# Kernel tuning notes

Measured on AMD Instinct MI355X. Metric: run time of the kernel, lower is better.

Reference implementation:

```python
import jax, jax.numpy as jnp
import numpy as np

N = 16384
D = 16          # chem_dims
K = 17          # knn k (first neighbor = self, dropped)
N_LAYERS = 3
NEG_SLOPE = 0.2
EPS = 1e-5


def group_norm(m, gamma, beta, groups=2, eps=EPS):
    # m: [N, C]; torch GroupNorm normalizes each row over each channel group
    n, c = m.shape
    g = m.reshape(n, groups, c // groups)
    mu = g.mean(-1, keepdims=True)
    var = ((g - mu) ** 2).mean(-1, keepdims=True)
    g = (g - mu) / jnp.sqrt(var + eps)
    return g.reshape(n, c) * gamma + beta


def setup_inputs() -> dict:
    key = jax.random.key(0)
    ks = jax.random.split(key, 8)
    x = jax.random.normal(ks[0], (N, 3), dtype=jnp.float32) * 10.0
    y = x  # atom-atom self graph: same point cloud
    y_atomtypes = jax.random.normal(ks[1], (N, D), dtype=jnp.float32)
    x_batch = jnp.sort(jax.random.randint(ks[2], (N,), 0, 4)).astype(jnp.int32)
    y_batch = x_batch
    Din = 2 * D + 1  # 33
    W1 = jax.random.normal(ks[3], (N_LAYERS, Din, Din), dtype=jnp.float32) * 0.1
    b1 = jnp.zeros((N_LAYERS, Din), dtype=jnp.float32)
    W2 = jax.random.normal(ks[4], (N_LAYERS, Din, D), dtype=jnp.float32) * 0.1
    b2 = jnp.zeros((N_LAYERS, D), dtype=jnp.float32)
    gamma = jnp.ones((N_LAYERS, D), dtype=jnp.float32)
    beta = jnp.zeros((N_LAYERS, D), dtype=jnp.float32)
    return {"x": x, "y": y, "y_atomtypes": y_atomtypes, "W1": W1, "b1": b1,
            "W2": W2, "b2": b2, "gamma": gamma, "beta": beta,
            "x_batch": x_batch, "y_batch": y_batch}


def knn(x, y, x_batch, y_batch, k):
    # brute-force batched KNN (keops argKmin equivalent)
    d2 = ((x * x).sum(-1)[:, None] + (y * y).sum(-1)[None, :]
          - 2.0 * x @ y.T)                                  # [N, N]
    d2 = jnp.where(x_batch[:, None] != y_batch[None, :], jnp.float32(1e30), d2)
    _, idx = jax.lax.top_k(-d2, k)                          # smallest distances
    return idx


def reference(x, y, y_atomtypes, W1, b1, W2, b2, gamma, beta, x_batch, y_batch):
    idx = knn(x, y, x_batch, y_batch, K)[:, 1:]             # drop self -> [N, K-1]
    nbr_xyz = y[idx]                                        # [N, k, 3]
    dists = ((x[:, None, :] - nbr_xyz) ** 2).sum(-1)        # [N, k]
    k = K - 1
    out = y_atomtypes
    for i in range(N_LAYERS):
        nbr = out[idx]                                      # [N, k, D] gather
        feat = jnp.concatenate(
            [jnp.broadcast_to(out[:, None, :], (out.shape[0], k, out.shape[1])),
             nbr, dists[..., None]], axis=-1)               # [N, k, 2D+1]
        h = jax.nn.leaky_relu(feat @ W1[i] + b1[i], NEG_SLOPE)
        messages = (h @ W2[i] + b2[i]).sum(1)               # sum over k -> [N, D]
        out = out + jax.nn.leaky_relu(group_norm(messages, gamma[i], beta[i]), NEG_SLOPE)
    return out
```

## Files before the change

### kernel.cpp

```cpp
#include <hip/hip_runtime.h>


#define N_PTS 16384
#define D 16
#define DIN 33
#define NEG 0.2f
#define GEPS 1e-5f
#define INFF 3.0e38f
#define SHRINK_AT 192

__global__ __launch_bounds__(256) void prep_kernel(const float* __restrict__ x,
                                                   float4* __restrict__ xyz4, int n) {
  int i = blockIdx.x * 256 + threadIdx.x;
  if (i < n) xyz4[i] = make_float4(x[3*i], x[3*i+1], x[3*i+2], 0.f);
}

__device__ __forceinline__ int pool_shrink(float* __restrict__ pd, int* __restrict__ pi,
                                           int pcount, float& tau, int l,
                                           unsigned long long lmask) {
  __asm__ volatile("s_waitcnt lgkmcnt(0)" ::: "memory");
  float e0 = INFF, e1 = INFF, e2 = INFF, e3 = INFF;
  int   j0 = 0, j1 = 0, j2 = 0, j3 = 0;
  const bool p0 = l < pcount, p1 = l + 64 < pcount, p2 = l + 128 < pcount, p3 = l + 192 < pcount;
  if (p0) { e0 = pd[l];       j0 = pi[l]; }
  if (p1) { e1 = pd[l + 64];  j1 = pi[l + 64]; }
  if (p2) { e2 = pd[l + 128]; j2 = pi[l + 128]; }
  if (p3) { e3 = pd[l + 192]; j3 = pi[l + 192]; }
  float mx = fmaxf(fmaxf(p0 ? e0 : 0.f, p1 ? e1 : 0.f), fmaxf(p2 ? e2 : 0.f, p3 ? e3 : 0.f));
#pragma unroll
  for (int m = 1; m < 64; m <<= 1) mx = fmaxf(mx, __shfl_xor(mx, m));
  float lo = 0.f, hi = mx * 1.000001f + 1e-35f;
  for (int it = 0; it < 12; ++it) {
    const float mid = 0.5f * (lo + hi);
    const int c = __popcll(__ballot(e0 < mid)) + __popcll(__ballot(e1 < mid))
                + __popcll(__ballot(e2 < mid)) + __popcll(__ballot(e3 < mid));
    if (c >= 16) hi = mid; else lo = mid;
  }
  tau = hi;
  int base = 0;
  { const bool k = e0 < tau; const unsigned long long m = __ballot(k);
    if (k) { const int pos = base + __popcll(m & lmask); pd[pos] = e0; pi[pos] = j0; }
    base += __popcll(m); }
  { const bool k = e1 < tau; const unsigned long long m = __ballot(k);
    if (k) { const int pos = base + __popcll(m & lmask); pd[pos] = e1; pi[pos] = j1; }
    base += __popcll(m); }
  { const bool k = e2 < tau; const unsigned long long m = __ballot(k);
    if (k) { const int pos = base + __popcll(m & lmask); pd[pos] = e2; pi[pos] = j2; }
    base += __popcll(m); }
  { const bool k = e3 < tau; const unsigned long long m = __ballot(k);
    if (k) { const int pos = base + __popcll(m & lmask); pd[pos] = e3; pi[pos] = j3; }
    base += __popcll(m); }
  return base;
}

__device__ __forceinline__ void pool_extract16(const float* __restrict__ pd,
                                               const int* __restrict__ pi,
                                               int pcount, int q, int l,
                                               int* __restrict__ knn_idx,
                                               float* __restrict__ knn_d2) {
  __asm__ volatile("s_waitcnt lgkmcnt(0)" ::: "memory");
  float e0 = INFF, e1 = INFF, e2 = INFF, e3 = INFF;
  int   j0 = -1 - l, j1 = -65 - l, j2 = -129 - l, j3 = -193 - l;
  if (l       < pcount) { e0 = pd[l];       j0 = pi[l]; }
  if (l + 64  < pcount) { e1 = pd[l + 64];  j1 = pi[l + 64]; }
  if (l + 128 < pcount) { e2 = pd[l + 128]; j2 = pi[l + 128]; }
  if (l + 192 < pcount) { e3 = pd[l + 192]; j3 = pi[l + 192]; }
  float rv = 0.f; int ri = q;
  for (int r = 0; r < 16; ++r) {
    float bv = e0; int bi = j0; int bs = 0;
    if (e1 < bv || (e1 == bv && j1 < bi)) { bv = e1; bi = j1; bs = 1; }
    if (e2 < bv || (e2 == bv && j2 < bi)) { bv = e2; bi = j2; bs = 2; }
    if (e3 < bv || (e3 == bv && j3 < bi)) { bv = e3; bi = j3; bs = 3; }
    const float lv = bv; const int li = bi;
#pragma unroll
    for (int m = 1; m < 64; m <<= 1) {
      const float ov = __shfl_xor(bv, m);
      const int   oi = __shfl_xor(bi, m);
      if (ov < bv || (ov == bv && oi < bi)) { bv = ov; bi = oi; }
    }
    if (lv == bv && li == bi) {
      if (bs == 0)      { e0 = INFF; j0 = -1 - l; }
      else if (bs == 1) { e1 = INFF; j1 = -65 - l; }
      else if (bs == 2) { e2 = INFF; j2 = -129 - l; }
      else              { e3 = INFF; j3 = -193 - l; }
    }
    if (l == r) { rv = bv; ri = bi; }
  }
  if (l < 16) {
    knn_idx[q * 16 + l] = ri;
    knn_d2 [q * 16 + l] = rv;
  }
}

__global__ __launch_bounds__(256) void knn_kernel(const float4* __restrict__ xyz4,
                                                  const int* __restrict__ batch,
                                                  int* __restrict__ knn_idx,
                                                  float* __restrict__ knn_d2, int n) {
  __shared__ float pd[4][256];
  __shared__ int   pi[4][256];
  const int tid = threadIdx.x;
  const int w = tid >> 6;
  const int l = tid & 63;
  const int q = blockIdx.x * 4 + w;

  const float4 Q = xyz4[q];
  const int b = batch[q];
  int lo, hi;
  { int a = 0, c = n; while (a < c) { int m = (a + c) >> 1; if (batch[m] <  b) a = m + 1; else c = m; } lo = a; }
  { int a = lo, c = n; while (a < c) { int m = (a + c) >> 1; if (batch[m] <= b) a = m + 1; else c = m; } hi = a; }

  const unsigned long long lmask = (1ull << l) - 1ull;
  float tau = INFF;
  int pcount = 0;

  for (int j0 = lo; j0 < hi; j0 += 64) {
    const int j = j0 + l;
    bool pass = false; float d2 = 0.f;
    if (j < hi) {
      const float4 P = xyz4[j];
      const float dx = Q.x - P.x, dy = Q.y - P.y, dz = Q.z - P.z;
      d2 = dx*dx + dy*dy + dz*dz;
      pass = (d2 < tau) && (j != q);
    }
    const unsigned long long m = __ballot(pass);
    if (m) {
      if (pass) {
        const int pos = pcount + __popcll(m & lmask);
        pd[w][pos] = d2; pi[w][pos] = j;
      }
      pcount += __popcll(m);
      if (pcount >= SHRINK_AT) {
        pcount = pool_shrink(&pd[w][0], &pi[w][0], pcount, tau, l, lmask);
      }
    }
  }
  pool_extract16(&pd[w][0], &pi[w][0], pcount, q, l, knn_idx, knn_d2);
}

__device__ __forceinline__ void load16(const float4* __restrict__ base, int row, float* dst) {
  float4 a = base[row*4+0], b = base[row*4+1], c = base[row*4+2], d = base[row*4+3];
  dst[0]=a.x;  dst[1]=a.y;  dst[2]=a.z;  dst[3]=a.w;
  dst[4]=b.x;  dst[5]=b.y;  dst[6]=b.z;  dst[7]=b.w;
  dst[8]=c.x;  dst[9]=c.y;  dst[10]=c.z; dst[11]=c.w;
  dst[12]=d.x; dst[13]=d.y; dst[14]=d.z; dst[15]=d.w;
}

__device__ __forceinline__ float lrelu(float x) {
  return fmaxf(x, 0.f) + NEG * fminf(x, 0.f);
}

__global__ __launch_bounds__(256) void layer_kernel(
    const float* __restrict__ in, const int* __restrict__ knn_idx,
    const float* __restrict__ knn_d2,
    const float* __restrict__ W1, const float* __restrict__ b1,
    const float* __restrict__ W2, const float* __restrict__ b2,
    const float* __restrict__ gamma, const float* __restrict__ beta,
    float* __restrict__ outb) {
  __shared__ float sW2[DIN * D];
  __shared__ float sb2[D], sg[D], sbt[D];
  const int tid = threadIdx.x;
  for (int t = tid; t < DIN * D; t += 256) sW2[t] = W2[t];
  if (tid < D) { sb2[tid] = b2[tid]; sg[tid] = gamma[tid]; sbt[tid] = beta[tid]; }
  __syncthreads();

  const int p = blockIdx.x * 16 + (tid >> 4);
  const int c = tid & 15;
  const float4* in4 = (const float4*)in;

  float s[16], nf[16];
  load16(in4, p, s);
  const int   nb = knn_idx[p * 16 + c];
  const float dk = knn_d2 [p * 16 + c];
  load16(in4, nb, nf);

  float h[DIN];
#pragma unroll
  for (int o = 0; o < DIN; ++o) h[o] = b1[o] + dk * W1[32 * DIN + o];
#pragma unroll
  for (int i = 0; i < 16; ++i) {
    const float si = s[i], ni = nf[i];
#pragma unroll
    for (int o = 0; o < DIN; ++o) {
      h[o] += si * W1[i * DIN + o];
      h[o] += ni * W1[(16 + i) * DIN + o];
    }
  }
#pragma unroll
  for (int o = 0; o < DIN; ++o) h[o] = lrelu(h[o]);

#pragma unroll
  for (int o = 0; o < DIN; ++o) {
    float x = h[o];
    x += __shfl_xor(x, 1);
    x += __shfl_xor(x, 2);
    x += __shfl_xor(x, 4);
    x += __shfl_xor(x, 8);
    h[o] = x;
  }

  float m = sb2[c];
#pragma unroll
  for (int i = 0; i < DIN; ++i) m += h[i] * sW2[i * D + c];

  float sum = m;
  sum += __shfl_xor(sum, 1); sum += __shfl_xor(sum, 2); sum += __shfl_xor(sum, 4);
  const float mu = sum * 0.125f;
  const float dd = m - mu;
  float sq = dd * dd;
  sq += __shfl_xor(sq, 1); sq += __shfl_xor(sq, 2); sq += __shfl_xor(sq, 4);
  const float var = sq * 0.125f;
  float yv = dd * (1.0f / sqrtf(var + GEPS));
  yv = yv * sg[c] + sbt[c];

  const float selfc = in[p * 16 + c];
  outb[p * 16 + c] = selfc + lrelu(yv);
}

extern "C" void kernel_launch(void* const* d_in, const int* in_sizes, int n_in,
                              void* d_out, int out_size, void* d_ws, size_t ws_size,
                              hipStream_t stream) {
  const float* x     = (const float*)d_in[0];
  const float* yat   = (const float*)d_in[2];
  const float* W1    = (const float*)d_in[3];
  const float* b1    = (const float*)d_in[4];
  const float* W2    = (const float*)d_in[5];
  const float* b2    = (const float*)d_in[6];
  const float* gamma = (const float*)d_in[7];
  const float* beta  = (const float*)d_in[8];
  const int*   xb    = (const int*)d_in[9];
  float* out = (float*)d_out;

  char* ws = (char*)d_ws;
  float4* xyz4 = (float4*)(ws);
  int*    kidx = (int*)  (ws + 262144);
  float*  kd2  = (float*)(ws + 262144 + 1048576);
  float*  bufA = (float*)(ws + 262144 + 2*1048576);
  float*  bufB = (float*)(ws + 262144 + 3*1048576);

  prep_kernel<<<N_PTS / 256, 256, 0, stream>>>(x, xyz4, N_PTS);
  knn_kernel<<<N_PTS / 4, 256, 0, stream>>>(xyz4, xb, kidx, kd2, N_PTS);
  layer_kernel<<<N_PTS / 16, 256, 0, stream>>>(yat,  kidx, kd2,
      W1 + 0*DIN*DIN, b1 + 0*DIN, W2 + 0*DIN*D, b2 + 0*D, gamma + 0*D, beta + 0*D, bufA);
  layer_kernel<<<N_PTS / 16, 256, 0, stream>>>(bufA, kidx, kd2,
      W1 + 1*DIN*DIN, b1 + 1*DIN, W2 + 1*DIN*D, b2 + 1*D, gamma + 1*D, beta + 1*D, bufB);
  layer_kernel<<<N_PTS / 16, 256, 0, stream>>>(bufB, kidx, kd2,
      W1 + 2*DIN*DIN, b1 + 2*DIN, W2 + 2*DIN*D, b2 + 2*D, gamma + 2*D, beta + 2*D, out);
}
```

Measured before the change: 234.3 us.

## Use integer-bit bisection for KNN selection and split layer work by output channel

```diff
diff --git a/kernel.cpp b/kernel.cpp
--- a/kernel.cpp
+++ b/kernel.cpp
@@ -7,6 +7,7 @@
 #define NEG 0.2f
 #define GEPS 1e-5f
 #define INFF 3.0e38f
+#define INFU 0x7f800000u
 #define SHRINK_AT 192
 
 __global__ __launch_bounds__(256) void prep_kernel(const float* __restrict__ x,
@@ -15,81 +16,98 @@
   if (i < n) xyz4[i] = make_float4(x[3*i], x[3*i+1], x[3*i+2], 0.f);
 }
 
+__device__ __forceinline__ unsigned bisect16(unsigned u0, unsigned u1,
+                                             unsigned u2, unsigned u3) {
+  unsigned lo = 0u, hi = 0x7f800001u;
+  for (int it = 0; it < 31; ++it) {
+    const unsigned mid = lo + ((hi - lo) >> 1);
+    const int c = __popcll(__ballot(u0 < mid)) + __popcll(__ballot(u1 < mid))
+                + __popcll(__ballot(u2 < mid)) + __popcll(__ballot(u3 < mid));
+    if (c >= 16) hi = mid; else lo = mid;
+  }
+  return lo;
+}
+
 __device__ __forceinline__ int pool_shrink(float* __restrict__ pd, int* __restrict__ pi,
                                            int pcount, float& tau, int l,
                                            unsigned long long lmask) {
   __asm__ volatile("s_waitcnt lgkmcnt(0)" ::: "memory");
-  float e0 = INFF, e1 = INFF, e2 = INFF, e3 = INFF;
-  int   j0 = 0, j1 = 0, j2 = 0, j3 = 0;
-  const bool p0 = l < pcount, p1 = l + 64 < pcount, p2 = l + 128 < pcount, p3 = l + 192 < pcount;
-  if (p0) { e0 = pd[l];       j0 = pi[l]; }
-  if (p1) { e1 = pd[l + 64];  j1 = pi[l + 64]; }
-  if (p2) { e2 = pd[l + 128]; j2 = pi[l + 128]; }
-  if (p3) { e3 = pd[l + 192]; j3 = pi[l + 192]; }
-  float mx = fmaxf(fmaxf(p0 ? e0 : 0.f, p1 ? e1 : 0.f), fmaxf(p2 ? e2 : 0.f, p3 ? e3 : 0.f));
-#pragma unroll
-  for (int m = 1; m < 64; m <<= 1) mx = fmaxf(mx, __shfl_xor(mx, m));
-  float lo = 0.f, hi = mx * 1.000001f + 1e-35f;
-  for (int it = 0; it < 12; ++it) {
-    const float mid = 0.5f * (lo + hi);
-    const int c = __popcll(__ballot(e0 < mid)) + __popcll(__ballot(e1 < mid))
-                + __popcll(__ballot(e2 < mid)) + __popcll(__ballot(e3 < mid));
-    if (c >= 16) hi = mid; else lo = mid;
-  }
-  tau = hi;
+  unsigned u0 = INFU, u1 = INFU, u2 = INFU, u3 = INFU;
+  int j0 = 0, j1 = 0, j2 = 0, j3 = 0;
+  if (l       < pcount) { u0 = __float_as_uint(pd[l]);       j0 = pi[l]; }
+  if (l + 64  < pcount) { u1 = __float_as_uint(pd[l + 64]);  j1 = pi[l + 64]; }
+  if (l + 128 < pcount) { u2 = __float_as_uint(pd[l + 128]); j2 = pi[l + 128]; }
+  if (l + 192 < pcount) { u3 = __float_as_uint(pd[l + 192]); j3 = pi[l + 192]; }
+  const unsigned t = bisect16(u0, u1, u2, u3);
+  tau = __uint_as_float(t);
   int base = 0;
-  { const bool k = e0 < tau; const unsigned long long m = __ballot(k);
-    if (k) { const int pos = base + __popcll(m & lmask); pd[pos] = e0; pi[pos] = j0; }
-    base += __popcll(m); }
-  { const bool k = e1 < tau; const unsigned long long m = __ballot(k);
-    if (k) { const int pos = base + __popcll(m & lmask); pd[pos] = e1; pi[pos] = j1; }
-    base += __popcll(m); }
-  { const bool k = e2 < tau; const unsigned long long m = __ballot(k);
-    if (k) { const int pos = base + __popcll(m & lmask); pd[pos] = e2; pi[pos] = j2; }
-    base += __popcll(m); }
-  { const bool k = e3 < tau; const unsigned long long m = __ballot(k);
-    if (k) { const int pos = base + __popcll(m & lmask); pd[pos] = e3; pi[pos] = j3; }
+  { const bool k = u0 <= t; const unsigned long long m = __ballot(k);
+    if (k) { const int pos = base + __popcll(m & lmask);
+             pd[pos] = __uint_as_float(u0); pi[pos] = j0; }
+    base += __popcll(m); }
+  { const bool k = u1 <= t; const unsigned long long m = __ballot(k);
+    if (k) { const int pos = base + __popcll(m & lmask);
+             pd[pos] = __uint_as_float(u1); pi[pos] = j1; }
+    base += __popcll(m); }
+  { const bool k = u2 <= t; const unsigned long long m = __ballot(k);
+    if (k) { const int pos = base + __popcll(m & lmask);
+             pd[pos] = __uint_as_float(u2); pi[pos] = j2; }
+    base += __popcll(m); }
+  { const bool k = u3 <= t; const unsigned long long m = __ballot(k);
+    if (k) { const int pos = base + __popcll(m & lmask);
+             pd[pos] = __uint_as_float(u3); pi[pos] = j3; }
     base += __popcll(m); }
   return base;
 }
 
-__device__ __forceinline__ void pool_extract16(const float* __restrict__ pd,
-                                               const int* __restrict__ pi,
-                                               int pcount, int q, int l,
-                                               int* __restrict__ knn_idx,
-                                               float* __restrict__ knn_d2) {
+__device__ __forceinline__ void pool_final16(const float* __restrict__ pd,
+                                             const int* __restrict__ pi,
+                                             int pcount, int q, int l,
+                                             int* __restrict__ knn_idx,
+                                             float* __restrict__ knn_d2) {
   __asm__ volatile("s_waitcnt lgkmcnt(0)" ::: "memory");
-  float e0 = INFF, e1 = INFF, e2 = INFF, e3 = INFF;
-  int   j0 = -1 - l, j1 = -65 - l, j2 = -129 - l, j3 = -193 - l;
-  if (l       < pcount) { e0 = pd[l];       j0 = pi[l]; }
-  if (l + 64  < pcount) { e1 = pd[l + 64];  j1 = pi[l + 64]; }
-  if (l + 128 < pcount) { e2 = pd[l + 128]; j2 = pi[l + 128]; }
-  if (l + 192 < pcount) { e3 = pd[l + 192]; j3 = pi[l + 192]; }
-  float rv = 0.f; int ri = q;
-  for (int r = 0; r < 16; ++r) {
-    float bv = e0; int bi = j0; int bs = 0;
-    if (e1 < bv || (e1 == bv && j1 < bi)) { bv = e1; bi = j1; bs = 1; }
-    if (e2 < bv || (e2 == bv && j2 < bi)) { bv = e2; bi = j2; bs = 2; }
-    if (e3 < bv || (e3 == bv && j3 < bi)) { bv = e3; bi = j3; bs = 3; }
-    const float lv = bv; const int li = bi;
-#pragma unroll
-    for (int m = 1; m < 64; m <<= 1) {
-      const float ov = __shfl_xor(bv, m);
-      const int   oi = __shfl_xor(bi, m);
-      if (ov < bv || (ov == bv && oi < bi)) { bv = ov; bi = oi; }
-    }
-    if (lv == bv && li == bi) {
-      if (bs == 0)      { e0 = INFF; j0 = -1 - l; }
-      else if (bs == 1) { e1 = INFF; j1 = -65 - l; }
-      else if (bs == 2) { e2 = INFF; j2 = -129 - l; }
-      else              { e3 = INFF; j3 = -193 - l; }
-    }
-    if (l == r) { rv = bv; ri = bi; }
-  }
-  if (l < 16) {
-    knn_idx[q * 16 + l] = ri;
-    knn_d2 [q * 16 + l] = rv;
-  }
+  const unsigned long long lmask = (1ull << l) - 1ull;
+  unsigned u0 = INFU, u1 = INFU, u2 = INFU, u3 = INFU;
+  int j0 = 0, j1 = 0, j2 = 0, j3 = 0;
+  if (l       < pcount) { u0 = __float_as_uint(pd[l]);       j0 = pi[l]; }
+  if (l + 64  < pcount) { u1 = __float_as_uint(pd[l + 64]);  j1 = pi[l + 64]; }
+  if (l + 128 < pcount) { u2 = __float_as_uint(pd[l + 128]); j2 = pi[l + 128]; }
+  if (l + 192 < pcount) { u3 = __float_as_uint(pd[l + 192]); j3 = pi[l + 192]; }
+  const unsigned t = bisect16(u0, u1, u2, u3);
+  int base = 0;
+  { const bool k = u0 < t; const unsigned long long m = __ballot(k);
+    if (k) { const int pos = base + __popcll(m & lmask);
+             knn_idx[q*16+pos] = j0; knn_d2[q*16+pos] = __uint_as_float(u0); }
+    base += __popcll(m); }
+  { const bool k = u1 < t; const unsigned long long m = __ballot(k);
+    if (k) { const int pos = base + __popcll(m & lmask);
+             knn_idx[q*16+pos] = j1; knn_d2[q*16+pos] = __uint_as_float(u1); }
+    base += __popcll(m); }
+  { const bool k = u2 < t; const unsigned long long m = __ballot(k);
+    if (k) { const int pos = base + __popcll(m & lmask);
+             knn_idx[q*16+pos] = j2; knn_d2[q*16+pos] = __uint_as_float(u2); }
+    base += __popcll(m); }
+  { const bool k = u3 < t; const unsigned long long m = __ballot(k);
+    if (k) { const int pos = base + __popcll(m & lmask);
+             knn_idx[q*16+pos] = j3; knn_d2[q*16+pos] = __uint_as_float(u3); }
+    base += __popcll(m); }
+  const float tf = __uint_as_float(t);
+  { const bool k = u0 == t; const unsigned long long m = __ballot(k);
+    if (k) { const int pos = base + __popcll(m & lmask);
+             if (pos < 16) { knn_idx[q*16+pos] = j0; knn_d2[q*16+pos] = tf; } }
+    base += __popcll(m); }
+  { const bool k = u1 == t; const unsigned long long m = __ballot(k);
+    if (k) { const int pos = base + __popcll(m & lmask);
+             if (pos < 16) { knn_idx[q*16+pos] = j1; knn_d2[q*16+pos] = tf; } }
+    base += __popcll(m); }
+  { const bool k = u2 == t; const unsigned long long m = __ballot(k);
+    if (k) { const int pos = base + __popcll(m & lmask);
+             if (pos < 16) { knn_idx[q*16+pos] = j2; knn_d2[q*16+pos] = tf; } }
+    base += __popcll(m); }
+  { const bool k = u3 == t; const unsigned long long m = __ballot(k);
+    if (k) { const int pos = base + __popcll(m & lmask);
+             if (pos < 16) { knn_idx[q*16+pos] = j3; knn_d2[q*16+pos] = tf; } }
+    base += __popcll(m); }
 }
 
 __global__ __launch_bounds__(256) void knn_kernel(const float4* __restrict__ xyz4,
@@ -134,7 +152,7 @@
       }
     }
   }
-  pool_extract16(&pd[w][0], &pi[w][0], pcount, q, l, knn_idx, knn_d2);
+  pool_final16(&pd[w][0], &pi[w][0], pcount, q, l, knn_idx, knn_d2);
 }
 
 __device__ __forceinline__ void load16(const float4* __restrict__ base, int row, float* dst) {
@@ -156,51 +174,65 @@
     const float* __restrict__ W2, const float* __restrict__ b2,
     const float* __restrict__ gamma, const float* __restrict__ beta,
     float* __restrict__ outb) {
-  __shared__ float sW2[DIN * D];
-  __shared__ float sb2[D], sg[D], sbt[D];
   const int tid = threadIdx.x;
-  for (int t = tid; t < DIN * D; t += 256) sW2[t] = W2[t];
-  if (tid < D) { sb2[tid] = b2[tid]; sg[tid] = gamma[tid]; sbt[tid] = beta[tid]; }
-  __syncthreads();
-
-  const int p = blockIdx.x * 16 + (tid >> 4);
+  const int g = tid >> 4;
   const int c = tid & 15;
+  const int p = blockIdx.x * 16 + g;
+
+  __shared__ float sH[16][36];
+
+  float w1a[DIN], w1b[DIN], w2c[DIN];
+#pragma unroll
+  for (int i = 0; i < DIN; ++i) {
+    w1a[i] = W1[i*DIN + c];
+    w1b[i] = W1[i*DIN + 16 + c];
+    w2c[i] = W2[i*D + c];
+  }
+  const float b1a = b1[c], b1b = b1[16 + c];
+
   const float4* in4 = (const float4*)in;
-
-  float s[16], nf[16];
+  float s[16];
   load16(in4, p, s);
-  const int   nb = knn_idx[p * 16 + c];
-  const float dk = knn_d2 [p * 16 + c];
-  load16(in4, nb, nf);
-
-  float h[DIN];
-#pragma unroll
-  for (int o = 0; o < DIN; ++o) h[o] = b1[o] + dk * W1[32 * DIN + o];
-#pragma unroll
-  for (int i = 0; i < 16; ++i) {
-    const float si = s[i], ni = nf[i];
-#pragma unroll
-    for (int o = 0; o < DIN; ++o) {
-      h[o] += si * W1[i * DIN + o];
-      h[o] += ni * W1[(16 + i) * DIN + o];
-    }
-  }
-#pragma unroll
-  for (int o = 0; o < DIN; ++o) h[o] = lrelu(h[o]);
-
-#pragma unroll
-  for (int o = 0; o < DIN; ++o) {
-    float x = h[o];
-    x += __shfl_xor(x, 1);
-    x += __shfl_xor(x, 2);
-    x += __shfl_xor(x, 4);
-    x += __shfl_xor(x, 8);
-    h[o] = x;
-  }
-
-  float m = sb2[c];
-#pragma unroll
-  for (int i = 0; i < DIN; ++i) m += h[i] * sW2[i * D + c];
+
+  const int*   kidx = knn_idx + p * 16;
+  const float* kd2  = knn_d2  + p * 16;
+
+  float hsA = 0.f, hsB = 0.f, hsZ = 0.f;
+#pragma unroll 2
+  for (int k = 0; k < 16; ++k) {
+    const int   nb = kidx[k];
+    const float dk = kd2[k];
+    float nf[16];
+    load16(in4, nb, nf);
+    float ha = b1a + dk * w1a[32];
+    float hb = b1b + dk * w1b[32];
+#pragma unroll
+    for (int i = 0; i < 16; ++i) {
+      ha += s[i]  * w1a[i];
+      ha += nf[i] * w1a[16 + i];
+      hb += s[i]  * w1b[i];
+      hb += nf[i] * w1b[16 + i];
+    }
+    hsA += lrelu(ha);
+    hsB += lrelu(hb);
+    if (c == 15) {
+      float hz = b1[32] + dk * W1[32*DIN + 32];
+#pragma unroll
+      for (int i = 0; i < 16; ++i) {
+        hz += s[i]  * W1[i*DIN + 32];
+        hz += nf[i] * W1[(16 + i)*DIN + 32];
+      }
+      hsZ += lrelu(hz);
+    }
+  }
+
+  sH[g][c]      = hsA;
+  sH[g][16 + c] = hsB;
+  if (c == 15) sH[g][32] = hsZ;
+
+  float m = b2[c];
+#pragma unroll
+  for (int i = 0; i < DIN; ++i) m += sH[g][i] * w2c[i];
 
   float sum = m;
   sum += __shfl_xor(sum, 1); sum += __shfl_xor(sum, 2); sum += __shfl_xor(sum, 4);
@@ -210,10 +242,9 @@
   sq += __shfl_xor(sq, 1); sq += __shfl_xor(sq, 2); sq += __shfl_xor(sq, 4);
   const float var = sq * 0.125f;
   float yv = dd * (1.0f / sqrtf(var + GEPS));
-  yv = yv * sg[c] + sbt[c];
-
-  const float selfc = in[p * 16 + c];
-  outb[p * 16 + c] = selfc + lrelu(yv);
+  yv = yv * gamma[c] + beta[c];
+
+  outb[p * 16 + c] = in[p * 16 + c] + lrelu(yv);
 }
 
 extern "C" void kernel_launch(void* const* d_in, const int* in_sizes, int n_in,
```

After: 266.3 us. 1.14x slower.
